# Optimization experiments

Measured on AMD Instinct MI355X. Metric: run time of the kernel, lower is better.

## Reference

```python
import jax, jax.numpy as jnp
import numpy as np
from jax.scipy.special import logsumexp

N = 16    # taxa
K = 128   # particles
S = 512   # sites (batch == full sites)
A = 4     # alphabet (DNA)
D = 64    # embedding dim
C = 16    # site-position encoding dim
PRIOR_BL = 1.0
RATE = 1.0 / PRIOR_BL


def _log_double_factorials(n_max):
    v = np.zeros(n_max + 1)
    for i in range(2, n_max + 1):
        v[i] = v[i - 2] + np.log(i)
    return jnp.asarray(v, dtype=jnp.float32)

LOG_DF = _log_double_factorials(2 * N)


def _gather_K(arr, idx):
    return arr[jnp.arange(arr.shape[0]), idx]


def _remove2(arr_t, i1, i2):
    # drop entries i1, i2 along leading axis, preserving order (static output size t-2)
    t = arr_t.shape[0]
    ar = jnp.arange(t)
    keep = (ar != i1) & (ar != i2)
    order = jnp.argsort(~keep)[: t - 2]  # stable sort: kept entries first, in order
    return arr_t[order]


def _merge_K(arr, i1, i2, new_K):
    # replace_with_merged_K: remove the two merged subtrees, append the new one
    removed = jax.vmap(_remove2)(arr, i1, i2)
    return jnp.concatenate([removed, new_K[:, None]], axis=1)


def _stat_probs(emb_VxD, siteC_SxC, W_stat, W_site):
    logits = (emb_VxD @ W_stat)[:, None, :] + (siteC_SxC @ W_site)[None]  # V,S,A
    return jax.nn.softmax(logits, axis=-1)


def _log_P_F81(stat_KxSxA, b_K):
    # F81 rate matrix Q = pi - I  =>  P(t) = e^{-t} I + (1 - e^{-t}) pi (closed-form expm)
    e = jnp.exp(-b_K)[:, None, None, None]
    P = e * jnp.eye(A, dtype=stat_KxSxA.dtype) + (1.0 - e) * stat_KxSxA[:, :, None, :]
    return jnp.log(P + 1e-30)  # K,S,A,A


def _fel_half(logP, log_fel):
    # logsumexp_b ( logP[k,s,a,b] + log_fel[k,s,b] )
    return logsumexp(logP + log_fel[:, :, None, :], axis=-1)


def _forward(data_NxSxA, data_batched_NxSxA, site_positions_SxSfull, W_enc, W_merge, W_stat, W_pos, W_site):
    key = jax.random.key(42)
    siteC = site_positions_SxSfull @ W_pos                      # S,C
    emb0 = jnp.tanh(data_NxSxA.reshape(N, -1) @ W_enc)          # N,D (seq_encoder)
    embeddings = jnp.broadcast_to(emb0[None], (K, N, D))
    log_fel = jnp.broadcast_to(jnp.log(data_batched_NxSxA)[None], (K, N, S, A))
    leaf_counts = jnp.ones((K, N), jnp.int32)
    merge1 = jnp.zeros((K, 0), jnp.int32)
    merge2 = jnp.zeros((K, 0), jnp.int32)
    br1 = jnp.zeros((K, 0), dtype=data_NxSxA.dtype)
    br2 = jnp.zeros((K, 0), dtype=data_NxSxA.dtype)
    log_pi = jnp.zeros(K)
    log_w = jnp.zeros(K)
    log_lik = jnp.zeros(K)
    log_ws = []
    log_rate = jnp.log(jnp.asarray(RATE, data_NxSxA.dtype))
    for r in range(N - 1):
        t = N - r
        key, k1, k2, k3, k4 = jax.random.split(key, 5)
        # ---- categorical resampling ----
        idxK = jax.random.categorical(k1, log_w, shape=(K,))
        merge1, merge2 = merge1[idxK], merge2[idxK]
        br1, br2 = br1[idxK], br2[idxK]
        leaf_counts = leaf_counts[idxK]
        embeddings = embeddings[idxK]
        log_fel = log_fel[idxK]
        log_pi, log_w = log_pi[idxK], log_w[idxK]
        # ---- proposal: uniform pair + exponential branch lengths ----
        i1s, i2s = np.triu_indices(t, 1)
        npairs = len(i1s)
        p = jax.random.randint(k2, (K,), 0, npairs)
        idx1 = jnp.asarray(i1s, jnp.int32)[p]
        idx2 = jnp.asarray(i2s, jnp.int32)[p]
        b1 = jax.random.exponential(k3, (K,)) * PRIOR_BL
        b2 = jax.random.exponential(k4, (K,)) * PRIOR_BL
        log_v_plus = -jnp.log(float(npairs)) + (log_rate - RATE * b1) + (log_rate - RATE * b2)
        log_v_minus = jnp.zeros(K)
        e1, e2 = _gather_K(embeddings, idx1), _gather_K(embeddings, idx2)
        new_emb = jnp.tanh(jnp.concatenate([e1, e2], axis=-1) @ W_merge)  # K,D
        # ---- record merge history (concat_K) ----
        merge1 = jnp.concatenate([merge1, idx1[:, None]], axis=1)
        merge2 = jnp.concatenate([merge2, idx2[:, None]], axis=1)
        br1 = jnp.concatenate([br1, b1[:, None]], axis=1)
        br2 = jnp.concatenate([br2, b2[:, None]], axis=1)
        new_lc = _gather_K(leaf_counts, idx1) + _gather_K(leaf_counts, idx2)
        f1, f2 = _gather_K(log_fel, idx1), _gather_K(log_fel, idx2)
        leaf_counts = _merge_K(leaf_counts, idx1, idx2, new_lc)
        embeddings = _merge_K(embeddings, idx1, idx2, new_emb)
        # ---- Felsenstein pruning step at the new internal node ----
        stat_new = _stat_probs(new_emb, siteC, W_stat, W_site)  # K,S,A
        new_fel = _fel_half(_log_P_F81(stat_new, b1), f1) + _fel_half(_log_P_F81(stat_new, b2), f2)
        log_fel = _merge_K(log_fel, idx1, idx2, new_fel)
        # ---- forest log-likelihood and log pi ----
        tn = t - 1
        stat_all = _stat_probs(embeddings.reshape(K * tn, D), siteC, W_stat, W_site)
        log_stat = jnp.log(stat_all).reshape(K, tn, S, A)
        log_lik = jnp.sum(logsumexp(log_fel + log_stat, axis=-1), axis=(1, 2))  # K
        log_top = -jnp.sum(LOG_DF[jnp.clip(2 * leaf_counts - 3, 0)], axis=1)
        log_branch = jnp.sum(log_rate - RATE * br1, axis=1) + jnp.sum(log_rate - RATE * br2, axis=1)
        prev_log_pi = log_pi
        log_pi = log_lik + log_top + log_branch
        log_w = log_pi - prev_log_pi + log_v_minus - log_v_plus
        log_ws.append(log_w)
    log_ws = jnp.stack(log_ws)  # (N-1), K
    log_Z_SMC = jnp.sum(logsumexp(log_ws - jnp.log(float(K)), axis=1))
    best = jnp.argmax(log_lik)
    return (log_Z_SMC, log_lik, merge1[best], merge2[best], br1[best], br2[best])


def setup_inputs() -> dict:
    key = jax.random.key(0)
    ks = jax.random.split(key, 6)
    data = jax.random.uniform(ks[0], (N, S, A), minval=0.05, maxval=1.0)
    return {
        "data_NxSxA": data,
        "data_batched_NxSxA": data,
        "site_positions_SxSfull": jnp.eye(S, dtype=jnp.float32),
        "W_enc": jax.random.normal(ks[1], (S * A, D)) / float(np.sqrt(S * A)),
        "W_merge": jax.random.normal(ks[2], (2 * D, D)) / float(np.sqrt(2 * D)),
        "W_stat": jax.random.normal(ks[3], (D, A)) / float(np.sqrt(D)),
        "W_pos": jax.random.normal(ks[4], (S, C)) / float(np.sqrt(S)),
        "W_site": jax.random.normal(ks[5], (C, A)) / float(np.sqrt(C)),
    }


def reference(data_NxSxA, data_batched_NxSxA, site_positions_SxSfull, W_enc, W_merge, W_stat, W_pos, W_site):
    return _forward(data_NxSxA, data_batched_NxSxA, site_positions_SxSfull, W_enc, W_merge, W_stat, W_pos, W_site)
```

## Files before the change

### kernel.cpp

```cpp
#include <hip/hip_runtime.h>
#include <stdint.h>


#define NN 16
#define KK 128
#define SS 512
#define NR 15
#define PARTITIONABLE 1
#define TINYF 1.17549435e-38f
#define NROWS (NN + NR * KK)

__host__ __device__ __forceinline__ void tf2x32(uint32_t k0, uint32_t k1,
                                                uint32_t c0, uint32_t c1,
                                                uint32_t* o0, uint32_t* o1) {
  uint32_t ks2 = k0 ^ k1 ^ 0x1BD11BDAu;
  uint32_t x0 = c0 + k0, x1 = c1 + k1;
  uint32_t ks[3] = {k0, k1, ks2};
  const uint32_t RA[4] = {13u, 15u, 26u, 6u};
  const uint32_t RB[4] = {17u, 29u, 16u, 24u};
#pragma unroll
  for (int i = 0; i < 5; ++i) {
#pragma unroll
    for (int j = 0; j < 4; ++j) {
      uint32_t r = (i & 1) ? RB[j] : RA[j];
      x0 += x1;
      x1 = (x1 << r) | (x1 >> (32u - r));
      x1 ^= x0;
    }
    x0 += ks[(i + 1) % 3];
    x1 += ks[(i + 2) % 3] + (uint32_t)(i + 1);
  }
  *o0 = x0; *o1 = x1;
}

__device__ __forceinline__ uint32_t rbits32(uint32_t ka, uint32_t kb,
                                            uint32_t i, uint32_t total) {
#if PARTITIONABLE
  uint32_t o0, o1;
  tf2x32(ka, kb, 0u, i, &o0, &o1);
  return o0 ^ o1;
#else
  uint32_t half = total >> 1;
  uint32_t o0, o1;
  if (i < half) { tf2x32(ka, kb, i, i + half, &o0, &o1); return o0; }
  tf2x32(ka, kb, i - half, i, &o0, &o1);
  return o1;
#endif
}

__device__ __forceinline__ float bits_unif(uint32_t b) {
  return __uint_as_float((b >> 9) | 0x3f800000u) - 1.0f;
}

__device__ __forceinline__ float xla_tanh(float x) {
  float ax = fabsf(x);
  float xc = fminf(fmaxf(x, -7.90531110763549805f), 7.90531110763549805f);
  float x2 = __fmul_rn(xc, xc);
  float num = -2.76076847742355e-16f;
  num = __fadd_rn(__fmul_rn(x2, num), 2.00018790482477e-13f);
  num = __fadd_rn(__fmul_rn(x2, num), -8.60467152213735e-11f);
  num = __fadd_rn(__fmul_rn(x2, num), 5.12229709037114e-08f);
  num = __fadd_rn(__fmul_rn(x2, num), 1.48572235717979e-05f);
  num = __fadd_rn(__fmul_rn(x2, num), 6.37261928875436e-04f);
  num = __fadd_rn(__fmul_rn(x2, num), 4.89352455891786e-03f);
  num = __fmul_rn(xc, num);
  float den = 1.19825839466702e-06f;
  den = __fadd_rn(__fmul_rn(x2, den), 1.18534705686654e-04f);
  den = __fadd_rn(__fmul_rn(x2, den), 2.26843463243900e-03f);
  den = __fadd_rn(__fmul_rn(x2, den), 4.89352518554385e-03f);
  float r = __fdiv_rn(num, den);
  return (ax < 0.0004f) ? x : r;
}

__device__ __forceinline__ float fin_or0(float v) {
  return (v > -INFINITY && v < INFINITY) ? v : 0.0f;
}

__device__ __forceinline__ void fold8(float& ll, const float4* b4, int n4) {
  if (n4 <= 0) return;
  float4 pre[8];
#pragma unroll
  for (int i = 0; i < 8; ++i) pre[i] = b4[i];
  for (int q = 8; q <= n4; q += 8) {
    float4 cur[8];
#pragma unroll
    for (int i = 0; i < 8; ++i) cur[i] = pre[i];
    if (q < n4) {
#pragma unroll
      for (int i = 0; i < 8; ++i) pre[i] = b4[q + i];
    }
#pragma unroll
    for (int i = 0; i < 8; ++i) {
      ll = __fadd_rn(ll, cur[i].x);
      ll = __fadd_rn(ll, cur[i].y);
      ll = __fadd_rn(ll, cur[i].z);
      ll = __fadd_rn(ll, cur[i].w);
    }
  }
}

__global__ void k_setup(const float* datab, const float* Wpos, const float* Wsite,
                        float* fel_pool, float* sitelog, float* logw0,
                        float* logpi0, int* lc_pool, int* ilist0, float* logdf) {
  int b = blockIdx.x, tid = threadIdx.x;
  if (b < 64) {
    int id = b * 256 + tid;
    fel_pool[id] = logf(datab[id]);
    fel_pool[16384 + id] = logf(datab[16384 + id]);
  } else if (b < 72) {
    int id = (b - 64) * 256 + tid;
    int s = id >> 2, aa = id & 3;
    float acc = 0.0f;
    for (int c = 0; c < 16; ++c) acc = fmaf(Wpos[s * 16 + c], Wsite[c * 4 + aa], acc);
    sitelog[id] = acc;
  } else {
    if (tid < KK) {
      logw0[tid] = 0.0f;
      logpi0[tid] = 0.0f;
      for (int nn2 = 0; nn2 < NN; ++nn2) ilist0[tid * 16 + nn2] = nn2;
    }
    if (tid < NN) lc_pool[tid] = 1;
    if (tid == 0) {
      double vv[33];
      vv[0] = 0.0; vv[1] = 0.0;
      for (int i = 2; i <= 32; ++i) vv[i] = vv[i - 2] + log((double)i);
      for (int i = 0; i < 33; ++i) logdf[i] = (float)vv[i];
    }
  }
}

__global__ __launch_bounds__(64) void k_emb0(const float* data, const float* Wenc,
                                             const float* Wstat, float* emb_pool,
                                             float* ew0) {
  int n = blockIdx.x, d = threadIdx.x;
  __shared__ float ne[64];
  const float* dp = data + n * 2048;
  const float* wp = Wenc + d;
  float acc = 0.0f;
#pragma unroll 32
  for (int i = 0; i < 2048; ++i) acc = fmaf(dp[i], wp[(size_t)i * 64], acc);
  float v = xla_tanh(acc);
  ne[d] = v;
  emb_pool[n * 64 + d] = v;
  __syncthreads();
  if (d < 4) {
    float s = 0.0f;
    for (int c = 0; c < 64; ++c) s = fmaf(ne[c], Wstat[c * 4 + d], s);
    ew0[n * 4 + d] = s;
  }
}

__global__ void k_leafterm(const float* fel_pool, const float* ew0,
                           const float* sitelog, float* st_pool) {
  int id = blockIdx.x * blockDim.x + threadIdx.x;
  if (id >= NN * SS) return;
  int n = id >> 9, s = id & 511;
  float lg[4], ex[4], stat[4];
  for (int a = 0; a < 4; ++a) lg[a] = __fadd_rn(ew0[n * 4 + a], sitelog[s * 4 + a]);
  float m = lg[0];
  for (int a = 1; a < 4; ++a) m = fmaxf(m, lg[a]);
  float ssum = 0.0f;
  for (int a = 0; a < 4; ++a) { ex[a] = expf(__fsub_rn(lg[a], m)); ssum = __fadd_rn(ssum, ex[a]); }
  for (int a = 0; a < 4; ++a) stat[a] = __fdiv_rn(ex[a], ssum);
  float q[4], am = -INFINITY;
  for (int a = 0; a < 4; ++a) {
    q[a] = __fadd_rn(fel_pool[n * 2048 + s * 4 + a], logf(stat[a]));
    am = fmaxf(am, q[a]);
  }
  am = fin_or0(am);
  float se = 0.0f;
  for (int a = 0; a < 4; ++a) se = __fadd_rn(se, expf(__fsub_rn(q[a], am)));
  st_pool[n * 512 + s] = __fadd_rn(logf(se), am);
}

__global__ __launch_bounds__(256) void k_round(
    uint32_t ka, uint32_t kb, uint32_t k2a, uint32_t k2b,
    uint32_t k3a, uint32_t k3b, uint32_t k4a, uint32_t k4b,
    int t, int r,
    const float* logwC, float* logwN,
    const float* logpiC, float* logpiN,
    const int* ilistC, int* ilistN,
    const int* m1C, int* m1N, const int* m2C, int* m2N,
    const float* br1C, float* br1N, const float* br2C, float* br2N,
    float* emb_pool, float* fel_pool, float* st_pool, int* lc_pool,
    const float* Wmerge, const float* Wstat, const float* sitelog,
    const float* logdf, float* logws_r, float* loglik) {
  int k = blockIdx.x, tid = threadIdx.x;
  int tn = t - 1, tn2 = t - 2;
  int newrow = NN + r * KK + k;
  __shared__ float stbuf[15 * 512];
  __shared__ float cat[128];
  __shared__ float ne[64];
  __shared__ float ewl[4];
  __shared__ float smax[4];
  __shared__ int sidx[4];
  __shared__ int sI1, sI2;
  __shared__ float sB1, sB2, sLvp, sE1, sE2;
  __shared__ int ilN[16];
  __shared__ int lcb[16];
  __shared__ float brb1[15], brb2[15];

  float v = -INFINITY;
  if (tid < 128) {
    uint32_t bits = rbits32(ka, kb, (uint32_t)(k * KK + tid), KK * KK);
    float f = bits_unif(bits);
    float u = fmaxf(TINYF, __fadd_rn(f, TINYF));
    float gv = -logf(-logf(u));
    v = __fadd_rn(gv, logwC[tid]);
  } else if (tid == 128) {
    uint32_t h = rbits32(k2a, k2b, (uint32_t)k, 256u);
    uint32_t l = rbits32(k2a, k2b, (uint32_t)(128 + k), 256u);
    uint32_t span = (uint32_t)(t * (t - 1) / 2);
    uint32_t mult = 65536u % span;
    mult = (mult * mult) % span;
    uint32_t off = ((h % span) * mult + (l % span)) % span;
    int p = (int)off;
    int a1 = 0, rem = p, rl = t - 1;
    while (rem >= rl) { rem -= rl; ++a1; --rl; }
    sI1 = a1;
    sI2 = a1 + 1 + rem;
    uint32_t bb = rbits32(k3a, k3b, (uint32_t)k, 128u);
    float e1 = -log1pf(-bits_unif(bb));
    bb = rbits32(k4a, k4b, (uint32_t)k, 128u);
    float e2 = -log1pf(-bits_unif(bb));
    sB1 = e1; sB2 = e2;
    float lnp = logf((float)span);
    sLvp = __fadd_rn(__fadd_rn(-lnp, -e1), -e2);
  }
  float m = v;
  for (int d = 32; d > 0; d >>= 1) m = fmaxf(m, __shfl_xor(m, d, 64));
  int w = tid >> 6;
  if ((tid & 63) == 0) smax[w] = m;
  __syncthreads();
  float gm = fmaxf(fmaxf(smax[0], smax[1]), fmaxf(smax[2], smax[3]));
  int cand = (v == gm) ? tid : 9999;
  for (int d = 32; d > 0; d >>= 1) {
    int o = __shfl_xor(cand, d, 64);
    cand = (o < cand) ? o : cand;
  }
  if ((tid & 63) == 0) sidx[w] = cand;
  __syncthreads();
  int a;
  {
    int b0 = (sidx[0] < sidx[1]) ? sidx[0] : sidx[1];
    int b1_ = (sidx[2] < sidx[3]) ? sidx[2] : sidx[3];
    a = (b0 < b1_) ? b0 : b1_;
  }
  int i1 = sI1, i2 = sI2;
  int p1 = ilistC[a * 16 + i1];
  int p2 = ilistC[a * 16 + i2];

  if (tid < 64) {
    cat[tid] = emb_pool[p1 * 64 + tid];
    cat[64 + tid] = emb_pool[p2 * 64 + tid];
  } else if (tid >= 64 && tid < 80) {
    int pos = tid - 64;
    if (pos < tn2) {
      int src = pos + (pos >= i1) + (pos >= (i2 - 1));
      int row = ilistC[a * 16 + src];
      ilN[pos] = row;
      ilistN[k * 16 + pos] = row;
      lcb[pos] = lc_pool[row];
    } else if (pos == tn2) {
      ilN[pos] = newrow;
      ilistN[k * 16 + pos] = newrow;
      int lcnew = lc_pool[p1] + lc_pool[p2];
      lcb[pos] = lcnew;
      lc_pool[newrow] = lcnew;
    }
  } else if (tid >= 96 && tid < 96 + NR) {
    int j = tid - 96;
    if (j < r) {
      int v1 = m1C[a * 15 + j]; m1N[k * 15 + j] = v1;
      int v2 = m2C[a * 15 + j]; m2N[k * 15 + j] = v2;
      float w1 = br1C[a * 15 + j]; br1N[k * 15 + j] = w1; brb1[j] = w1;
      float w2 = br2C[a * 15 + j]; br2N[k * 15 + j] = w2; brb2[j] = w2;
    } else if (j == r) {
      m1N[k * 15 + r] = i1;
      m2N[k * 15 + r] = i2;
      br1N[k * 15 + r] = sB1;
      br2N[k * 15 + r] = sB2;
      brb1[r] = sB1;
      brb2[r] = sB2;
    }
  } else if (tid == 128) {
    sE1 = expf(-sB1);
  } else if (tid == 129) {
    sE2 = expf(-sB2);
  }
  __syncthreads();

  if (tid < 64) {
    float acc = 0.0f;
    for (int c = 0; c < 128; ++c) acc = fmaf(cat[c], Wmerge[c * 64 + tid], acc);
    float vv = xla_tanh(acc);
    ne[tid] = vv;
    emb_pool[newrow * 64 + tid] = vv;
  } else {
    int nf4 = tn2 * 128;
    int base = tid - 64;
    float4 tmp[10];
#pragma unroll
    for (int it = 0; it < 10; ++it) {
      int q = base + it * 192;
      if (q < nf4)
        tmp[it] = *(const float4*)(st_pool + (size_t)ilN[q >> 7] * 512 + ((q & 127) << 2));
    }
#pragma unroll
    for (int it = 0; it < 10; ++it) {
      int q = base + it * 192;
      if (q < nf4) ((float4*)stbuf)[q] = tmp[it];
    }
  }
  __syncthreads();

  if (tid < 4) {
    float s = 0.0f;
    for (int c = 0; c < 64; ++c) s = fmaf(ne[c], Wstat[c * 4 + tid], s);
    ewl[tid] = s;
  }
  __syncthreads();

  float ll = 0.0f;
  if (tid == 0) {
    fold8(ll, (const float4*)stbuf, tn2 * 128);
  } else if (tid >= 64) {
    float e1 = sE1, e2 = sE2;
    float om1 = __fsub_rn(1.0f, e1), om2 = __fsub_rn(1.0f, e2);
    float ewv[4];
#pragma unroll
    for (int aa = 0; aa < 4; ++aa) ewv[aa] = ewl[aa];
    for (int s = tid - 64; s < 512; s += 192) {
      float lg[4], ex[4], stat[4];
#pragma unroll
      for (int aa = 0; aa < 4; ++aa) lg[aa] = __fadd_rn(ewv[aa], sitelog[s * 4 + aa]);
      float mm = lg[0];
#pragma unroll
      for (int aa = 1; aa < 4; ++aa) mm = fmaxf(mm, lg[aa]);
      float ssum = 0.0f;
#pragma unroll
      for (int aa = 0; aa < 4; ++aa) {
        ex[aa] = expf(__fsub_rn(lg[aa], mm));
        ssum = __fadd_rn(ssum, ex[aa]);
      }
#pragma unroll
      for (int aa = 0; aa < 4; ++aa) stat[aa] = __fdiv_rn(ex[aa], ssum);
      float4 f1v = *(const float4*)(fel_pool + (size_t)p1 * 2048 + s * 4);
      float4 f2v = *(const float4*)(fel_pool + (size_t)p2 * 2048 + s * 4);
      float f1a[4] = {f1v.x, f1v.y, f1v.z, f1v.w};
      float f2a[4] = {f2v.x, f2v.y, f2v.z, f2v.w};
      float lo1[4], ld1[4], lo2[4], ld2[4];
#pragma unroll
      for (int bb = 0; bb < 4; ++bb) {
        float m1v = __fmul_rn(om1, stat[bb]);
        lo1[bb] = logf(__fadd_rn(m1v, 1e-30f));
        ld1[bb] = logf(__fadd_rn(__fadd_rn(e1, m1v), 1e-30f));
        float m2v = __fmul_rn(om2, stat[bb]);
        lo2[bb] = logf(__fadd_rn(m2v, 1e-30f));
        ld2[bb] = logf(__fadd_rn(__fadd_rn(e2, m2v), 1e-30f));
      }
      float nf[4];
#pragma unroll
      for (int aa = 0; aa < 4; ++aa) {
        float q1[4], am = -INFINITY;
#pragma unroll
        for (int bb = 0; bb < 4; ++bb) {
          q1[bb] = __fadd_rn((aa == bb) ? ld1[bb] : lo1[bb], f1a[bb]);
          am = fmaxf(am, q1[bb]);
        }
        am = fin_or0(am);
        float se = 0.0f;
#pragma unroll
        for (int bb = 0; bb < 4; ++bb) se = __fadd_rn(se, expf(__fsub_rn(q1[bb], am)));
        float h1 = __fadd_rn(logf(se), am);
        float q2[4], am2 = -INFINITY;
#pragma unroll
        for (int bb = 0; bb < 4; ++bb) {
          q2[bb] = __fadd_rn((aa == bb) ? ld2[bb] : lo2[bb], f2a[bb]);
          am2 = fmaxf(am2, q2[bb]);
        }
        am2 = fin_or0(am2);
        float se2 = 0.0f;
#pragma unroll
        for (int bb = 0; bb < 4; ++bb) se2 = __fadd_rn(se2, expf(__fsub_rn(q2[bb], am2)));
        float h2 = __fadd_rn(logf(se2), am2);
        nf[aa] = __fadd_rn(h1, h2);
      }
      *(float4*)(fel_pool + (size_t)newrow * 2048 + s * 4) =
          make_float4(nf[0], nf[1], nf[2], nf[3]);
      float q3[4], am3 = -INFINITY;
#pragma unroll
      for (int aa = 0; aa < 4; ++aa) {
        q3[aa] = __fadd_rn(nf[aa], logf(stat[aa]));
        am3 = fmaxf(am3, q3[aa]);
      }
      am3 = fin_or0(am3);
      float se3 = 0.0f;
#pragma unroll
      for (int aa = 0; aa < 4; ++aa) se3 = __fadd_rn(se3, expf(__fsub_rn(q3[aa], am3)));
      float stv = __fadd_rn(logf(se3), am3);
      stbuf[tn2 * 512 + s] = stv;
      st_pool[(size_t)newrow * 512 + s] = stv;
    }
  }
  __syncthreads();

  if (tid == 0) {
    fold8(ll, (const float4*)(stbuf + tn2 * 512), 128);
    float lt = 0.0f;
    for (int pos = 0; pos < tn; ++pos) {
      int idx = 2 * lcb[pos] - 3;
      if (idx < 0) idx = 0;
      lt = __fadd_rn(lt, logdf[idx]);
    }
    lt = -lt;
    float s1 = 0.0f, s2 = 0.0f;
    for (int j = 0; j <= r; ++j) {
      s1 = __fadd_rn(s1, -brb1[j]);
      s2 = __fadd_rn(s2, -brb2[j]);
    }
    float lb = __fadd_rn(s1, s2);
    float lpi = __fadd_rn(__fadd_rn(ll, lt), lb);
    float prev = logpiC[a];
    float lw = __fsub_rn(__fadd_rn(__fsub_rn(lpi, prev), 0.0f), sLvp);
    logpiN[k] = lpi;
    logwN[k] = lw;
    logws_r[k] = lw;
    loglik[k] = ll;
  }
}

__global__ void k_final(const float* logws, const float* loglik,
                        const int* m1D, const int* m2D,
                        const float* br1D, const float* br2D, float* out) {
  int j = threadIdx.x;
  out[1 + j] = loglik[j];
  __shared__ float sm[2];
  __shared__ float ssum[2];
  __shared__ int si[2];
  float c = logf(128.0f);
  float z = 0.0f;
  for (int r = 0; r < NR; ++r) {
    float v = __fsub_rn(logws[r * KK + j], c);
    float m = v;
    for (int d = 32; d > 0; d >>= 1) m = fmaxf(m, __shfl_xor(m, d, 64));
    if ((j & 63) == 0) sm[j >> 6] = m;
    __syncthreads();
    float gm = fin_or0(fmaxf(sm[0], sm[1]));
    float e = expf(__fsub_rn(v, gm));
    for (int d = 32; d > 0; d >>= 1) e = __fadd_rn(e, __shfl_xor(e, d, 64));
    if ((j & 63) == 0) ssum[j >> 6] = e;
    __syncthreads();
    if (j == 0) z = __fadd_rn(z, __fadd_rn(logf(__fadd_rn(ssum[0], ssum[1])), gm));
    __syncthreads();
  }
  if (j == 0) out[0] = z;
  float lv = loglik[j];
  float m2 = lv;
  for (int d = 32; d > 0; d >>= 1) m2 = fmaxf(m2, __shfl_xor(m2, d, 64));
  if ((j & 63) == 0) sm[j >> 6] = m2;
  __syncthreads();
  float gm2 = fmaxf(sm[0], sm[1]);
  int cand = (lv == gm2) ? j : 9999;
  for (int d = 32; d > 0; d >>= 1) {
    int o = __shfl_xor(cand, d, 64);
    cand = (o < cand) ? o : cand;
  }
  if ((j & 63) == 0) si[j >> 6] = cand;
  __syncthreads();
  int bi = (si[0] < si[1]) ? si[0] : si[1];
  if (j < NR) {
    out[129 + j] = (float)m1D[bi * 15 + j];
    out[144 + j] = (float)m2D[bi * 15 + j];
    out[159 + j] = br1D[bi * 15 + j];
    out[174 + j] = br2D[bi * 15 + j];
  }
}

static void split5_host(uint32_t* key0, uint32_t* key1, uint32_t out[8]) {
#if PARTITIONABLE
  uint32_t nk0, nk1, o0, o1;
  tf2x32(*key0, *key1, 0u, 0u, &nk0, &nk1);
  for (int j = 1; j < 5; ++j) {
    tf2x32(*key0, *key1, 0u, (uint32_t)j, &o0, &o1);
    out[2 * (j - 1)] = o0;
    out[2 * (j - 1) + 1] = o1;
  }
  *key0 = nk0; *key1 = nk1;
#else
  uint32_t a0[5], a1[5];
  for (int i = 0; i < 5; ++i) tf2x32(*key0, *key1, (uint32_t)i, (uint32_t)(i + 5), &a0[i], &a1[i]);
  uint32_t flat[10] = {a0[0], a0[1], a0[2], a0[3], a0[4], a1[0], a1[1], a1[2], a1[3], a1[4]};
  *key0 = flat[0]; *key1 = flat[1];
  for (int j = 0; j < 8; ++j) out[j] = flat[2 + j];
#endif
}

extern "C" void kernel_launch(void* const* d_in, const int* in_sizes, int n_in,
                              void* d_out, int out_size, void* d_ws, size_t ws_size,
                              hipStream_t stream) {
  const float* data = (const float*)d_in[0];
  const float* datab = (const float*)d_in[1];
  const float* Wenc = (const float*)d_in[3];
  const float* Wmerge = (const float*)d_in[4];
  const float* Wstat = (const float*)d_in[5];
  const float* Wpos = (const float*)d_in[6];
  const float* Wsite = (const float*)d_in[7];
  float* out = (float*)d_out;

  char* base = (char*)d_ws;
  size_t off = 0;
  auto alloc = [&](size_t bytes) -> void* {
    void* p = base + off;
    off += (bytes + 255) & ~(size_t)255;
    return p;
  };
  float* fel_pool = (float*)alloc((size_t)NROWS * 2048 * 4);
  float* st_pool = (float*)alloc((size_t)NROWS * 512 * 4);
  float* emb_pool = (float*)alloc((size_t)NROWS * 64 * 4);
  int* lc_pool = (int*)alloc((size_t)NROWS * 4);
  int* ilist[2]; int* m1[2]; int* m2[2]; float* br1[2]; float* br2[2];
  float* logpi[2]; float* logw2[2];
  for (int b = 0; b < 2; ++b) ilist[b] = (int*)alloc((size_t)KK * 16 * 4);
  for (int b = 0; b < 2; ++b) m1[b] = (int*)alloc((size_t)KK * 15 * 4);
  for (int b = 0; b < 2; ++b) m2[b] = (int*)alloc((size_t)KK * 15 * 4);
  for (int b = 0; b < 2; ++b) br1[b] = (float*)alloc((size_t)KK * 15 * 4);
  for (int b = 0; b < 2; ++b) br2[b] = (float*)alloc((size_t)KK * 15 * 4);
  for (int b = 0; b < 2; ++b) logpi[b] = (float*)alloc((size_t)KK * 4);
  for (int b = 0; b < 2; ++b) logw2[b] = (float*)alloc((size_t)KK * 4);
  float* logws = (float*)alloc(NR * KK * 4);
  float* loglik = (float*)alloc(KK * 4);
  float* sitelog = (float*)alloc(SS * 4 * 4);
  float* logdf = (float*)alloc(33 * 4);
  float* ew0 = (float*)alloc(NN * 4 * 4);
  (void)ws_size; (void)in_sizes; (void)n_in; (void)out_size;

  k_setup<<<73, 256, 0, stream>>>(datab, Wpos, Wsite, fel_pool, sitelog,
                                  logw2[0], logpi[0], lc_pool, ilist[0], logdf);
  k_emb0<<<NN, 64, 0, stream>>>(data, Wenc, Wstat, emb_pool, ew0);
  k_leafterm<<<32, 256, 0, stream>>>(fel_pool, ew0, sitelog, st_pool);

  uint32_t key0 = 0u, key1 = 42u;
  for (int r = 0; r < NR; ++r) {
    uint32_t ks[8];
    split5_host(&key0, &key1, ks);
    int t = NN - r;
    int cur = r & 1, nxt = cur ^ 1;
    k_round<<<KK, 256, 0, stream>>>(
        ks[0], ks[1], ks[2], ks[3], ks[4], ks[5], ks[6], ks[7], t, r,
        logw2[cur], logw2[nxt], logpi[cur], logpi[nxt],
        ilist[cur], ilist[nxt], m1[cur], m1[nxt], m2[cur], m2[nxt],
        br1[cur], br1[nxt], br2[cur], br2[nxt],
        emb_pool, fel_pool, st_pool, lc_pool,
        Wmerge, Wstat, sitelog, logdf, logws + r * KK, loglik);
  }
  k_final<<<1, 128, 0, stream>>>(logws, loglik, m1[1], m2[1], br1[1], br2[1], out);
}
```

Measured before the change: 504.2 us.

## Precompute all-round RNG draws in setup and stage fel/sitelog in shared memory

Moves the per-round Gumbel, merge-index and branch-length random draws out of the serial k_round kernels into one wide parallel pass inside k_setup, so each round only loads precomputed values. Also stages the two child felsenstein rows and the sitelog table into shared memory alongside the st gather, folds the ewl computation into the embedding branch to remove one barrier, and unrolls the site loop. This shortens the critical path of the 15 dependent round launches, at the cost of a larger setup kernel, extra global scratch buffers and more shared memory per block.

```diff
diff --git a/kernel.cpp b/kernel.cpp
--- a/kernel.cpp
+++ b/kernel.cpp
@@ -99,9 +99,14 @@
   }
 }
 
-__global__ void k_setup(const float* datab, const float* Wpos, const float* Wsite,
-                        float* fel_pool, float* sitelog, float* logw0,
-                        float* logpi0, int* lc_pool, int* ilist0, float* logdf) {
+struct KeysAll { uint32_t v[NR][8]; };
+
+__global__ void k_setup(KeysAll keys, const float* datab, const float* Wpos,
+                        const float* Wsite, float* fel_pool, float* sitelog,
+                        float* logw0, float* logpi0, int* lc_pool, int* ilist0,
+                        float* logdf, float* gtab, int* pidx1, int* pidx2,
+                        float* pb1, float* pb2, float* plvp, float* pee1,
+                        float* pee2) {
   int b = blockIdx.x, tid = threadIdx.x;
   if (b < 64) {
     int id = b * 256 + tid;
@@ -113,7 +118,7 @@
     float acc = 0.0f;
     for (int c = 0; c < 16; ++c) acc = fmaf(Wpos[s * 16 + c], Wsite[c * 4 + aa], acc);
     sitelog[id] = acc;
-  } else {
+  } else if (b == 72) {
     if (tid < KK) {
       logw0[tid] = 0.0f;
       logpi0[tid] = 0.0f;
@@ -125,6 +130,40 @@
       vv[0] = 0.0; vv[1] = 0.0;
       for (int i = 2; i <= 32; ++i) vv[i] = vv[i - 2] + log((double)i);
       for (int i = 0; i < 33; ++i) logdf[i] = (float)vv[i];
+    }
+  } else if (b < 1033) {
+    int gi = (b - 73) * 256 + tid;
+    int r = gi >> 14;
+    uint32_t rem = (uint32_t)(gi & 16383);
+    uint32_t bits = rbits32(keys.v[r][0], keys.v[r][1], rem, KK * KK);
+    float f = bits_unif(bits);
+    float u = fmaxf(TINYF, __fadd_rn(f, TINYF));
+    gtab[gi] = -logf(-logf(u));
+  } else {
+    int gi = (b - 1033) * 256 + tid;
+    if (gi < NR * KK) {
+      int r = gi >> 7, k = gi & 127;
+      int t = NN - r;
+      uint32_t h = rbits32(keys.v[r][2], keys.v[r][3], (uint32_t)k, 256u);
+      uint32_t l = rbits32(keys.v[r][2], keys.v[r][3], (uint32_t)(128 + k), 256u);
+      uint32_t span = (uint32_t)(t * (t - 1) / 2);
+      uint32_t mult = 65536u % span;
+      mult = (mult * mult) % span;
+      uint32_t off = ((h % span) * mult + (l % span)) % span;
+      int p = (int)off;
+      int a1 = 0, rem = p, rl = t - 1;
+      while (rem >= rl) { rem -= rl; ++a1; --rl; }
+      pidx1[gi] = a1;
+      pidx2[gi] = a1 + 1 + rem;
+      uint32_t bb = rbits32(keys.v[r][4], keys.v[r][5], (uint32_t)k, 128u);
+      float e1 = -log1pf(-bits_unif(bb));
+      bb = rbits32(keys.v[r][6], keys.v[r][7], (uint32_t)k, 128u);
+      float e2 = -log1pf(-bits_unif(bb));
+      pb1[gi] = e1; pb2[gi] = e2;
+      float lnp = logf((float)span);
+      plvp[gi] = __fadd_rn(__fadd_rn(-lnp, -e1), -e2);
+      pee1[gi] = expf(-e1);
+      pee2[gi] = expf(-e2);
     }
   }
 }
@@ -173,10 +212,11 @@
   st_pool[n * 512 + s] = __fadd_rn(logf(se), am);
 }
 
-__global__ __launch_bounds__(256) void k_round(
-    uint32_t ka, uint32_t kb, uint32_t k2a, uint32_t k2b,
-    uint32_t k3a, uint32_t k3b, uint32_t k4a, uint32_t k4b,
+__global__ __launch_bounds__(256, 1) void k_round(
     int t, int r,
+    const float* gtab, const int* pidx1, const int* pidx2,
+    const float* pb1, const float* pb2, const float* plvp,
+    const float* pee1, const float* pee2,
     const float* logwC, float* logwN,
     const float* logpiC, float* logpiN,
     const int* ilistC, int* ilistN,
@@ -189,6 +229,8 @@
   int tn = t - 1, tn2 = t - 2;
   int newrow = NN + r * KK + k;
   __shared__ float stbuf[15 * 512];
+  __shared__ float felb[2][2048];
+  __shared__ float slb[2048];
   __shared__ float cat[128];
   __shared__ float ne[64];
   __shared__ float ewl[4];
@@ -202,30 +244,16 @@
 
   float v = -INFINITY;
   if (tid < 128) {
-    uint32_t bits = rbits32(ka, kb, (uint32_t)(k * KK + tid), KK * KK);
-    float f = bits_unif(bits);
-    float u = fmaxf(TINYF, __fadd_rn(f, TINYF));
-    float gv = -logf(-logf(u));
-    v = __fadd_rn(gv, logwC[tid]);
+    v = __fadd_rn(gtab[((size_t)r * KK + k) * KK + tid], logwC[tid]);
   } else if (tid == 128) {
-    uint32_t h = rbits32(k2a, k2b, (uint32_t)k, 256u);
-    uint32_t l = rbits32(k2a, k2b, (uint32_t)(128 + k), 256u);
-    uint32_t span = (uint32_t)(t * (t - 1) / 2);
-    uint32_t mult = 65536u % span;
-    mult = (mult * mult) % span;
-    uint32_t off = ((h % span) * mult + (l % span)) % span;
-    int p = (int)off;
-    int a1 = 0, rem = p, rl = t - 1;
-    while (rem >= rl) { rem -= rl; ++a1; --rl; }
-    sI1 = a1;
-    sI2 = a1 + 1 + rem;
-    uint32_t bb = rbits32(k3a, k3b, (uint32_t)k, 128u);
-    float e1 = -log1pf(-bits_unif(bb));
-    bb = rbits32(k4a, k4b, (uint32_t)k, 128u);
-    float e2 = -log1pf(-bits_unif(bb));
-    sB1 = e1; sB2 = e2;
-    float lnp = logf((float)span);
-    sLvp = __fadd_rn(__fadd_rn(-lnp, -e1), -e2);
+    int gi = r * KK + k;
+    sI1 = pidx1[gi];
+    sI2 = pidx2[gi];
+    sB1 = pb1[gi];
+    sB2 = pb2[gi];
+    sLvp = plvp[gi];
+    sE1 = pee1[gi];
+    sE2 = pee2[gi];
   }
   float m = v;
   for (int d = 32; d > 0; d >>= 1) m = fmaxf(m, __shfl_xor(m, d, 64));
@@ -283,10 +311,6 @@
       brb1[r] = sB1;
       brb2[r] = sB2;
     }
-  } else if (tid == 128) {
-    sE1 = expf(-sB1);
-  } else if (tid == 129) {
-    sE2 = expf(-sB2);
   }
   __syncthreads();
 
@@ -296,28 +320,49 @@
     float vv = xla_tanh(acc);
     ne[tid] = vv;
     emb_pool[newrow * 64 + tid] = vv;
+    if (tid < 4) {
+      float s = 0.0f;
+      for (int c = 0; c < 64; ++c) s = fmaf(ne[c], Wstat[c * 4 + tid], s);
+      ewl[tid] = s;
+    }
   } else {
     int nf4 = tn2 * 128;
     int base = tid - 64;
-    float4 tmp[10];
+    float4 tst[10], tf[6], tsl[3];
+    const float4* f1g = (const float4*)(fel_pool + (size_t)p1 * 2048);
+    const float4* f2g = (const float4*)(fel_pool + (size_t)p2 * 2048);
+    const float4* slg = (const float4*)sitelog;
 #pragma unroll
     for (int it = 0; it < 10; ++it) {
       int q = base + it * 192;
       if (q < nf4)
-        tmp[it] = *(const float4*)(st_pool + (size_t)ilN[q >> 7] * 512 + ((q & 127) << 2));
+        tst[it] = *(const float4*)(st_pool + (size_t)ilN[q >> 7] * 512 + ((q & 127) << 2));
+    }
+#pragma unroll
+    for (int it = 0; it < 6; ++it) {
+      int q = base + it * 192;
+      if (q < 1024) tf[it] = (q < 512) ? f1g[q] : f2g[q - 512];
+    }
+#pragma unroll
+    for (int it = 0; it < 3; ++it) {
+      int q = base + it * 192;
+      if (q < 512) tsl[it] = slg[q];
     }
 #pragma unroll
     for (int it = 0; it < 10; ++it) {
       int q = base + it * 192;
-      if (q < nf4) ((float4*)stbuf)[q] = tmp[it];
-    }
-  }
-  __syncthreads();
-
-  if (tid < 4) {
-    float s = 0.0f;
-    for (int c = 0; c < 64; ++c) s = fmaf(ne[c], Wstat[c * 4 + tid], s);
-    ewl[tid] = s;
+      if (q < nf4) ((float4*)stbuf)[q] = tst[it];
+    }
+#pragma unroll
+    for (int it = 0; it < 6; ++it) {
+      int q = base + it * 192;
+      if (q < 1024) ((float4*)felb)[q] = tf[it];
+    }
+#pragma unroll
+    for (int it = 0; it < 3; ++it) {
+      int q = base + it * 192;
+      if (q < 512) ((float4*)slb)[q] = tsl[it];
+    }
   }
   __syncthreads();
 
@@ -330,10 +375,12 @@
     float ewv[4];
 #pragma unroll
     for (int aa = 0; aa < 4; ++aa) ewv[aa] = ewl[aa];
-    for (int s = tid - 64; s < 512; s += 192) {
+    auto do_site = [&](int s) {
+      float4 slv = ((const float4*)slb)[s];
+      float sla[4] = {slv.x, slv.y, slv.z, slv.w};
       float lg[4], ex[4], stat[4];
 #pragma unroll
-      for (int aa = 0; aa < 4; ++aa) lg[aa] = __fadd_rn(ewv[aa], sitelog[s * 4 + aa]);
+      for (int aa = 0; aa < 4; ++aa) lg[aa] = __fadd_rn(ewv[aa], sla[aa]);
       float mm = lg[0];
 #pragma unroll
       for (int aa = 1; aa < 4; ++aa) mm = fmaxf(mm, lg[aa]);
@@ -345,8 +392,8 @@
       }
 #pragma unroll
       for (int aa = 0; aa < 4; ++aa) stat[aa] = __fdiv_rn(ex[aa], ssum);
-      float4 f1v = *(const float4*)(fel_pool + (size_t)p1 * 2048 + s * 4);
-      float4 f2v = *(const float4*)(fel_pool + (size_t)p2 * 2048 + s * 4);
+      float4 f1v = ((const float4*)felb[0])[s];
+      float4 f2v = ((const float4*)felb[1])[s];
       float f1a[4] = {f1v.x, f1v.y, f1v.z, f1v.w};
       float f2a[4] = {f2v.x, f2v.y, f2v.z, f2v.w};
       float lo1[4], ld1[4], lo2[4], ld2[4];
@@ -401,7 +448,11 @@
       float stv = __fadd_rn(logf(se3), am3);
       stbuf[tn2 * 512 + s] = stv;
       st_pool[(size_t)newrow * 512 + s] = stv;
-    }
+    };
+    int s0 = tid - 64;
+    do_site(s0);
+    do_site(s0 + 192);
+    if (s0 < 128) do_site(s0 + 384);
   }
   __syncthreads();
 
@@ -533,21 +584,31 @@
   float* sitelog = (float*)alloc(SS * 4 * 4);
   float* logdf = (float*)alloc(33 * 4);
   float* ew0 = (float*)alloc(NN * 4 * 4);
+  float* gtab = (float*)alloc((size_t)NR * KK * KK * 4);
+  int* pidx1 = (int*)alloc((size_t)NR * KK * 4);
+  int* pidx2 = (int*)alloc((size_t)NR * KK * 4);
+  float* pb1 = (float*)alloc((size_t)NR * KK * 4);
+  float* pb2 = (float*)alloc((size_t)NR * KK * 4);
+  float* plvp = (float*)alloc((size_t)NR * KK * 4);
+  float* pee1 = (float*)alloc((size_t)NR * KK * 4);
+  float* pee2 = (float*)alloc((size_t)NR * KK * 4);
   (void)ws_size; (void)in_sizes; (void)n_in; (void)out_size;
 
-  k_setup<<<73, 256, 0, stream>>>(datab, Wpos, Wsite, fel_pool, sitelog,
-                                  logw2[0], logpi[0], lc_pool, ilist[0], logdf);
+  KeysAll keys;
+  uint32_t key0 = 0u, key1 = 42u;
+  for (int r = 0; r < NR; ++r) split5_host(&key0, &key1, keys.v[r]);
+
+  k_setup<<<1041, 256, 0, stream>>>(keys, datab, Wpos, Wsite, fel_pool, sitelog,
+                                    logw2[0], logpi[0], lc_pool, ilist[0], logdf,
+                                    gtab, pidx1, pidx2, pb1, pb2, plvp, pee1, pee2);
   k_emb0<<<NN, 64, 0, stream>>>(data, Wenc, Wstat, emb_pool, ew0);
   k_leafterm<<<32, 256, 0, stream>>>(fel_pool, ew0, sitelog, st_pool);
 
-  uint32_t key0 = 0u, key1 = 42u;
   for (int r = 0; r < NR; ++r) {
-    uint32_t ks[8];
-    split5_host(&key0, &key1, ks);
     int t = NN - r;
     int cur = r & 1, nxt = cur ^ 1;
     k_round<<<KK, 256, 0, stream>>>(
-        ks[0], ks[1], ks[2], ks[3], ks[4], ks[5], ks[6], ks[7], t, r,
+        t, r, gtab, pidx1, pidx2, pb1, pb2, plvp, pee1, pee2,
         logw2[cur], logw2[nxt], logpi[cur], logpi[nxt],
         ilist[cur], ilist[nxt], m1[cur], m1[nxt], m2[cur], m2[nxt],
         br1[cur], br1[nxt], br2[cur], br2[nxt],
```

New measurement: 627.8 us. +24.5%, slower.
